# Optimization experiments

Hardware: AMD Instinct MI355X
Metric: run time of the kernel (lower is better)

## Reference

```python
import jax, jax.numpy as jnp
import numpy as np

B, S, C, O, H = 4, 4096, 2048, 2048, 8
DH = O // H  # per-head dim = 256
EPS = 1e-5


def setup_inputs() -> dict:
    key = jax.random.key(0)
    ks = jax.random.split(key, 12)
    init = lambda k, shape: (jax.random.normal(k, shape, dtype=jnp.float32) * 0.02)
    return {
        "x": jax.random.normal(ks[0], (B, S, C), dtype=jnp.float32),
        "Wq": init(ks[1], (C, O)), "bq": jnp.zeros((O,), jnp.float32),
        "Wk": init(ks[2], (C, O)), "bk": jnp.zeros((O,), jnp.float32),
        "Wv": init(ks[3], (C, O)), "bv": jnp.zeros((O,), jnp.float32),
        "Wo": init(ks[4], (O, C)), "bo": jnp.zeros((C,), jnp.float32),
        "gamma": jnp.ones((C,), jnp.float32),
        "beta": jnp.zeros((C,), jnp.float32),
    }


def reference(x, Wq, bq, Wk, bk, Wv, bv, Wo, bo, gamma, beta):
    b, s, _ = x.shape
    q = (x @ Wq + bq).reshape(b, s, H, DH)
    k = (x @ Wk + bk).reshape(b, s, H, DH)
    v = (x @ Wv + bv).reshape(b, s, H, DH)
    # As written in the source: matmul over the LAST two dims of [B,S,H,DH],
    # i.e. per-position attention across heads -> scores [B,S,H,H].
    scores = jnp.einsum("bshd,bstd->bsht", q, k) / jnp.sqrt(jnp.float32(DH))
    attn = jax.nn.softmax(scores, axis=-1)
    attended = jnp.einsum("bsht,bstd->bshd", attn, v).reshape(b, s, O)
    out = attended @ Wo + bo
    # residual + LayerNorm over the channel dim
    y = x + out
    mu = jnp.mean(y, axis=-1, keepdims=True)
    var = jnp.mean(jnp.square(y - mu), axis=-1, keepdims=True)
    return gamma * (y - mu) * jax.lax.rsqrt(var + EPS) + beta
```

## Files before the change

### kernel.cpp

```cpp
#include <hip/hip_runtime.h>
#include <hip/hip_bf16.h>
#include <stdint.h>


using short8  = __attribute__((ext_vector_type(8))) short;
using floatx4 = __attribute__((ext_vector_type(4))) float;

__device__ __forceinline__ float bf2f(ushort u) {
    union { uint32_t i; float f; } v; v.i = ((uint32_t)u) << 16; return v.f;
}
__device__ __forceinline__ ushort f2bf(float f) {
    union { float f; uint32_t i; } v; v.f = f;
    uint32_t r = v.i + 0x7fffu + ((v.i >> 16) & 1u);
    return (ushort)(r >> 16);
}
__device__ __forceinline__ short8 pack8(const floatx4& a, const floatx4& b) {
    short8 o;
    o[0] = (short)f2bf(a[0]); o[1] = (short)f2bf(a[1]);
    o[2] = (short)f2bf(a[2]); o[3] = (short)f2bf(a[3]);
    o[4] = (short)f2bf(b[0]); o[5] = (short)f2bf(b[1]);
    o[6] = (short)f2bf(b[2]); o[7] = (short)f2bf(b[3]);
    return o;
}
__device__ __forceinline__ void async_copy16(const void* g, void* l) {
    __builtin_amdgcn_global_load_lds(
        (__attribute__((address_space(1))) uint32_t*)g,
        (__attribute__((address_space(3))) uint32_t*)l,
        16, 0, 0);
}

#define GBAR do { asm volatile("" ::: "memory"); \
                  __builtin_amdgcn_s_barrier(); \
                  asm volatile("" ::: "memory"); } while (0)
#define LGKM0 asm volatile("s_waitcnt lgkmcnt(0)" ::: "memory")

__global__ void cvt_bf16(const float* __restrict__ in, ushort* __restrict__ out) {
    const size_t base = ((size_t)blockIdx.x * 256 + threadIdx.x) * 8;
    floatx4 a = *(const floatx4*)&in[base];
    floatx4 b = *(const floatx4*)&in[base + 4];
    *(short8*)&out[base] = pack8(a, b);
}

__global__ void convT2048(const float* __restrict__ in, ushort* __restrict__ out) {
    __shared__ alignas(16) float tile[32][33];
    const int x = blockIdx.x * 32 + threadIdx.x;
    const int y0 = blockIdx.y * 32;
    for (int j = threadIdx.y; j < 32; j += 8)
        tile[j][threadIdx.x] = in[(size_t)(y0 + j) * 2048 + x];
    __syncthreads();
    const int x2 = blockIdx.y * 32 + threadIdx.x;
    const int y2 = blockIdx.x * 32;
    for (int j = threadIdx.y; j < 32; j += 8)
        out[(size_t)(y2 + j) * 2048 + x2] = f2bf(tile[threadIdx.x][j]);
}

template <typename CT, int N>
__global__ __launch_bounds__(512, 2)
void gemm256(const ushort* __restrict__ A, int lda,
             const ushort* __restrict__ Bt,
             const float* __restrict__ b0, const float* __restrict__ b1,
             const float* __restrict__ b2,
             const float* __restrict__ resid, CT* __restrict__ C)
{
    constexpr int K   = 2048;
    constexpr int NKT = K / 64;
    constexpr int NT  = N / 256;
    constexpr int SW  = NT / 8;
    __shared__ alignas(16) ushort lA[2][256 * 64];
    __shared__ alignas(16) ushort lB[2][256 * 64];

    const int t    = threadIdx.x;
    const int wid  = t >> 6, lane = t & 63;
    const int wr   = wid >> 2, wc = wid & 3;
    const int lr   = lane & 15, q4 = lane >> 4;
    const int swk  = lr & 7;

    const int l    = (int)blockIdx.x;
    const int xcd  = l & 7;
    const int j2   = l >> 3;
    const int row0 = (j2 / SW) * 256;
    const int col0 = (xcd * SW + (j2 % SW)) * 256;

    const float* bias; int boff;
    if (col0 < 2048)      { bias = b0; boff = 0; }
    else if (col0 < 4096) { bias = b1; boff = 2048; }
    else                  { bias = b2; boff = 4096; }

    const int rpb = t >> 3;
    const int sp  = t & 7;
    const int gc0 = (sp ^ (rpb & 7)) * 8;
    const ushort* pA0 = A  + (size_t)(row0 + rpb)      * lda + gc0;
    const ushort* pA1 = A  + (size_t)(row0 + 64 + rpb) * lda + gc0;
    const ushort* pB0 = Bt + (size_t)(col0 + rpb)      * K   + gc0;
    const ushort* pB1 = Bt + (size_t)(col0 + 64 + rpb) * K   + gc0;

#define STAGE_A(buf, half, kn) do { \
    async_copy16(pA0 + (size_t)(half) * 128 * lda + (kn) * 64, \
                 &lA[buf][(half) * 8192 + t * 8]); \
    async_copy16(pA1 + (size_t)(half) * 128 * lda + (kn) * 64, \
                 &lA[buf][(half) * 8192 + 4096 + t * 8]); \
} while (0)
#define STAGE_B(buf, half, kn) do { \
    async_copy16(pB0 + (size_t)(half) * 128 * K + (kn) * 64, \
                 &lB[buf][(half) * 8192 + t * 8]); \
    async_copy16(pB1 + (size_t)(half) * 128 * K + (kn) * 64, \
                 &lB[buf][(half) * 8192 + 4096 + t * 8]); \
} while (0)

    const int arow = (wr * 128 + lr) * 64;
    const int brow = (wc * 64  + lr) * 64;
    const int c0 = ((0 + q4) ^ swk) * 8;
    const int c1 = ((4 + q4) ^ swk) * 8;

    floatx4 acc[8][4];
    #pragma unroll
    for (int i = 0; i < 8; i++)
        #pragma unroll
        for (int j = 0; j < 4; j++)
            acc[i][j] = (floatx4){0.f, 0.f, 0.f, 0.f};

    STAGE_A(0, 0, 0); STAGE_A(0, 1, 0);
    STAGE_B(0, 0, 0); STAGE_B(0, 1, 0);
    STAGE_A(1, 0, 1); STAGE_A(1, 1, 1);
    asm volatile("s_waitcnt vmcnt(4)" ::: "memory");
    GBAR;

    short8 af[8][2], bf[4][2];

    for (int kt = 0; kt < NKT; ++kt) {
        const int c = kt & 1;

        #pragma unroll
        for (int i = 0; i < 4; i++) {
            af[i][0] = *(const short8*)&lA[c][arow + i * 1024 + c0];
            af[i][1] = *(const short8*)&lA[c][arow + i * 1024 + c1];
        }
        #pragma unroll
        for (int j = 0; j < 2; j++) {
            bf[j][0] = *(const short8*)&lB[c][brow + j * 1024 + c0];
            bf[j][1] = *(const short8*)&lB[c][brow + j * 1024 + c1];
        }
        if (kt < NKT - 1) STAGE_B(c ^ 1, 0, kt + 1);
        GBAR; LGKM0;
        __builtin_amdgcn_s_setprio(1);
        #pragma unroll
        for (int i = 0; i < 4; i++)
            #pragma unroll
            for (int j = 0; j < 2; j++)
                #pragma unroll
                for (int ks = 0; ks < 2; ks++)
                    acc[i][j] = __builtin_amdgcn_mfma_f32_16x16x32_bf16(
                        af[i][ks], bf[j][ks], acc[i][j], 0, 0, 0);
        __builtin_amdgcn_s_setprio(0);
        GBAR;

        #pragma unroll
        for (int i = 4; i < 8; i++) {
            af[i][0] = *(const short8*)&lA[c][arow + i * 1024 + c0];
            af[i][1] = *(const short8*)&lA[c][arow + i * 1024 + c1];
        }
        #pragma unroll
        for (int j = 2; j < 4; j++) {
            bf[j][0] = *(const short8*)&lB[c][brow + j * 1024 + c0];
            bf[j][1] = *(const short8*)&lB[c][brow + j * 1024 + c1];
        }
        if (kt < NKT - 1) STAGE_B(c ^ 1, 1, kt + 1);
        GBAR; LGKM0;
        __builtin_amdgcn_s_setprio(1);
        #pragma unroll
        for (int i = 4; i < 8; i++)
            #pragma unroll
            for (int j = 2; j < 4; j++)
                #pragma unroll
                for (int ks = 0; ks < 2; ks++)
                    acc[i][j] = __builtin_amdgcn_mfma_f32_16x16x32_bf16(
                        af[i][ks], bf[j][ks], acc[i][j], 0, 0, 0);
        __builtin_amdgcn_s_setprio(0);
        GBAR;

        if (kt < NKT - 2) STAGE_A(c, 0, kt + 2);
        __builtin_amdgcn_s_setprio(1);
        #pragma unroll
        for (int i = 0; i < 4; i++)
            #pragma unroll
            for (int j = 2; j < 4; j++)
                #pragma unroll
                for (int ks = 0; ks < 2; ks++)
                    acc[i][j] = __builtin_amdgcn_mfma_f32_16x16x32_bf16(
                        af[i][ks], bf[j][ks], acc[i][j], 0, 0, 0);
        __builtin_amdgcn_s_setprio(0);
        GBAR;

        if (kt < NKT - 2) STAGE_A(c, 1, kt + 2);
        __builtin_amdgcn_s_setprio(1);
        #pragma unroll
        for (int i = 4; i < 8; i++)
            #pragma unroll
            for (int j = 0; j < 2; j++)
                #pragma unroll
                for (int ks = 0; ks < 2; ks++)
                    acc[i][j] = __builtin_amdgcn_mfma_f32_16x16x32_bf16(
                        af[i][ks], bf[j][ks], acc[i][j], 0, 0, 0);
        __builtin_amdgcn_s_setprio(0);
        if (kt < NKT - 2)       { asm volatile("s_waitcnt vmcnt(4)" ::: "memory"); }
        else if (kt == NKT - 2) { asm volatile("s_waitcnt vmcnt(0)" ::: "memory"); }
        if (kt < NKT - 1) GBAR;
    }
#undef STAGE_A
#undef STAGE_B

    #pragma unroll
    for (int j = 0; j < 4; j++) {
        const int gcol = col0 + wc * 64 + j * 16 + lr;
        const float bv = bias[gcol - boff];
        #pragma unroll
        for (int i = 0; i < 8; i++) {
            #pragma unroll
            for (int r = 0; r < 4; r++) {
                const int grow = row0 + wr * 128 + i * 16 + q4 * 4 + r;
                const size_t off = (size_t)grow * N + gcol;
                float v = acc[i][j][r] + bv;
                if (resid) v += resid[off];
                if constexpr (__is_same(CT, float)) C[off] = v;
                else                                C[off] = f2bf(v);
            }
        }
    }
}

template <int N>
__global__ __launch_bounds__(256, 2)
void gemm_f32a(const float* __restrict__ A, int lda,
               const ushort* __restrict__ Bt,
               const float* __restrict__ b0, const float* __restrict__ b1,
               const float* __restrict__ b2, ushort* __restrict__ C)
{
    constexpr int K = 2048;
    constexpr int NT = N / 128;
    constexpr int SW = NT / 8;
    __shared__ alignas(16) float  lA32[128 * 32];
    __shared__ alignas(16) ushort lB[128 * 32];

    const int t = threadIdx.x;
    const int wave = t >> 6, lane = t & 63;

    const int l = (int)blockIdx.x;
    const int xcd = l & 7;
    const int j2 = l >> 3;
    const int row0 = (j2 / SW) * 128;
    const int col0 = (xcd * SW + (j2 % SW)) * 128;

    const float* bias; int boff;
    if (col0 < 2048)      { bias = b0; boff = 0; }
    else if (col0 < 4096) { bias = b1; boff = 2048; }
    else                  { bias = b2; boff = 4096; }

    const int ar = t >> 3, ac = (t & 7) * 4;
    const float* gA0 = A + (size_t)(row0 + ar) * lda + ac;
    const ushort* gB0 = Bt + (size_t)(col0 + (t >> 2)) * K + (t & 3) * 8;
    const ushort* gB1 = Bt + (size_t)(col0 + 64 + (t >> 2)) * K + (t & 3) * 8;

    const int wm = (wave >> 1) * 64;
    const int wn = (wave & 1) * 64;
    const int q4 = lane >> 4;
    const int lr = lane & 15;

    floatx4 acc[4][4];
    #pragma unroll
    for (int i = 0; i < 4; i++)
        #pragma unroll
        for (int j = 0; j < 4; j++)
            acc[i][j] = (floatx4){0.f, 0.f, 0.f, 0.f};

    for (int kt = 0; kt < K / 32; ++kt) {
        const int ko = kt * 32;
        #pragma unroll
        for (int n = 0; n < 4; n++)
            async_copy16(gA0 + (size_t)n * 32 * lda + ko, &lA32[(n * 256 + t) * 4]);
        async_copy16(gB0 + ko, &lB[t * 8]);
        async_copy16(gB1 + ko, &lB[2048 + t * 8]);
        __syncthreads();

        short8 af[4], bfr[4];
        #pragma unroll
        for (int i = 0; i < 4; i++) {
            const floatx4* pa = (const floatx4*)&lA32[(wm + i * 16 + lr) * 32 + q4 * 8];
            af[i] = pack8(pa[0], pa[1]);
        }
        #pragma unroll
        for (int j = 0; j < 4; j++)
            bfr[j] = *(const short8*)&lB[(wn + j * 16 + lr) * 32 + q4 * 8];

        #pragma unroll
        for (int i = 0; i < 4; i++)
            #pragma unroll
            for (int j = 0; j < 4; j++)
                acc[i][j] = __builtin_amdgcn_mfma_f32_16x16x32_bf16(
                    af[i], bfr[j], acc[i][j], 0, 0, 0);
        __syncthreads();
    }

    #pragma unroll
    for (int j = 0; j < 4; j++) {
        const int gcol = col0 + wn + j * 16 + lr;
        const float bv = bias[gcol - boff];
        #pragma unroll
        for (int i = 0; i < 4; i++)
            #pragma unroll
            for (int r = 0; r < 4; r++) {
                const int grow = row0 + wm + i * 16 + q4 * 4 + r;
                C[(size_t)grow * N + gcol] = f2bf(acc[i][j][r] + bv);
            }
    }
}

__global__ __launch_bounds__(256, 2)
void attn_kernel(ushort* __restrict__ qkv)
{
    __shared__ alignas(16) ushort sq[4][2048];
    __shared__ alignas(16) ushort sk[4][2048];
    __shared__ alignas(16) ushort sv[4][2048];
    const int wave = threadIdx.x >> 6, lane = threadIdx.x & 63;
    const size_t p = (size_t)blockIdx.x * 4 + wave;
    const size_t base = p * 6144;

    #pragma unroll
    for (int c = 0; c < 4; c++) {
        const int idx = c * 512 + lane * 8;
        *(short8*)&sq[wave][idx] = *(const short8*)&qkv[base + idx];
        *(short8*)&sk[wave][idx] = *(const short8*)&qkv[base + 2048 + idx];
        *(short8*)&sv[wave][idx] = *(const short8*)&qkv[base + 4096 + idx];
    }

    const int h = lane >> 3;
    const int tt = lane & 7;
    float s = 0.f;
    #pragma unroll 4
    for (int c = 0; c < 32; c++) {
        short8 qv = *(const short8*)&sq[wave][h * 256 + c * 8];
        short8 kv = *(const short8*)&sk[wave][tt * 256 + c * 8];
        #pragma unroll
        for (int e = 0; e < 8; e++)
            s += bf2f((ushort)qv[e]) * bf2f((ushort)kv[e]);
    }
    s *= (1.0f / 16.0f);

    float m = s;
    m = fmaxf(m, __shfl_xor(m, 1));
    m = fmaxf(m, __shfl_xor(m, 2));
    m = fmaxf(m, __shfl_xor(m, 4));
    float e = __expf(s - m);
    float sum = e;
    sum += __shfl_xor(sum, 1);
    sum += __shfl_xor(sum, 2);
    sum += __shfl_xor(sum, 4);
    const float w = e / sum;

    float wt[8];
    #pragma unroll
    for (int t2 = 0; t2 < 8; t2++)
        wt[t2] = __shfl(w, (lane & 56) + t2);

    const int d0 = (lane & 7) * 8;
    #pragma unroll
    for (int c = 0; c < 4; c++) {
        const int d = d0 + c * 64;
        float acc[8] = {0, 0, 0, 0, 0, 0, 0, 0};
        #pragma unroll
        for (int t2 = 0; t2 < 8; t2++) {
            short8 vv = *(const short8*)&sv[wave][t2 * 256 + d];
            #pragma unroll
            for (int e2 = 0; e2 < 8; e2++)
                acc[e2] += wt[t2] * bf2f((ushort)vv[e2]);
        }
        short8 o;
        #pragma unroll
        for (int e2 = 0; e2 < 8; e2++)
            o[e2] = (short)f2bf(acc[e2]);
        *(short8*)&qkv[base + h * 256 + d] = o;
    }
}

__global__ __launch_bounds__(256, 2)
void ln_kernel(float* __restrict__ y, const float* __restrict__ gamma,
               const float* __restrict__ beta)
{
    __shared__ float red[2][4];
    const int t = threadIdx.x;
    const size_t base = (size_t)blockIdx.x * 2048 + t * 8;
    floatx4 a = *(const floatx4*)&y[base];
    floatx4 b = *(const floatx4*)&y[base + 4];
    float f[8] = {a[0], a[1], a[2], a[3], b[0], b[1], b[2], b[3]};
    float s = 0.f, ss = 0.f;
    #pragma unroll
    for (int e = 0; e < 8; e++) { s += f[e]; ss += f[e] * f[e]; }
    #pragma unroll
    for (int off = 1; off < 64; off <<= 1) {
        s  += __shfl_xor(s, off);
        ss += __shfl_xor(ss, off);
    }
    const int wave = t >> 6, lane = t & 63;
    if (lane == 0) { red[0][wave] = s; red[1][wave] = ss; }
    __syncthreads();
    s  = red[0][0] + red[0][1] + red[0][2] + red[0][3];
    ss = red[1][0] + red[1][1] + red[1][2] + red[1][3];
    const float mu  = s * (1.f / 2048.f);
    const float var = fmaxf(ss * (1.f / 2048.f) - mu * mu, 0.f);
    const float rs  = rsqrtf(var + 1e-5f);
    floatx4 g0 = *(const floatx4*)&gamma[t * 8];
    floatx4 g1 = *(const floatx4*)&gamma[t * 8 + 4];
    floatx4 b0 = *(const floatx4*)&beta[t * 8];
    floatx4 b1 = *(const floatx4*)&beta[t * 8 + 4];
    floatx4 o0, o1;
    #pragma unroll
    for (int e = 0; e < 4; e++) {
        o0[e] = g0[e] * (f[e] - mu) * rs + b0[e];
        o1[e] = g1[e] * (f[e + 4] - mu) * rs + b1[e];
    }
    *(floatx4*)&y[base]     = o0;
    *(floatx4*)&y[base + 4] = o1;
}

extern "C" void kernel_launch(void* const* d_in, const int* in_sizes, int n_in,
                              void* d_out, int out_size, void* d_ws, size_t ws_size,
                              hipStream_t stream)
{
    const float* x     = (const float*)d_in[0];
    const float* Wq    = (const float*)d_in[1];
    const float* bq    = (const float*)d_in[2];
    const float* Wk    = (const float*)d_in[3];
    const float* bk    = (const float*)d_in[4];
    const float* Wv    = (const float*)d_in[5];
    const float* bv    = (const float*)d_in[6];
    const float* Wo    = (const float*)d_in[7];
    const float* bo    = (const float*)d_in[8];
    const float* gamma = (const float*)d_in[9];
    const float* beta  = (const float*)d_in[10];
    float* out = (float*)d_out;

    char* ws = (char*)d_ws;
    const size_t MB = 1024 * 1024;
    ushort* WqkvT = (ushort*)(ws + 0 * MB);
    ushort* WoT   = (ushort*)(ws + 24 * MB);

    const bool bigws = ws_size >= 288 * MB;
    ushort* xbf = (ushort*)(ws + 32 * MB);
    ushort* qkv = (ushort*)(ws + (bigws ? 96 : 32) * MB);

    dim3 tb(32, 8), tg(64, 64);
    convT2048<<<tg, tb, 0, stream>>>(Wq, WqkvT);
    convT2048<<<tg, tb, 0, stream>>>(Wk, WqkvT + 2048 * 2048);
    convT2048<<<tg, tb, 0, stream>>>(Wv, WqkvT + 2 * 2048 * 2048);
    convT2048<<<tg, tb, 0, stream>>>(Wo, WoT);

    if (bigws) {
        cvt_bf16<<<16384, 256, 0, stream>>>(x, xbf);
        gemm256<ushort, 6144><<<1536, 512, 0, stream>>>(
            xbf, 2048, WqkvT, bq, bk, bv, nullptr, qkv);
    } else {
        gemm_f32a<6144><<<6144, 256, 0, stream>>>(
            x, 2048, WqkvT, bq, bk, bv, qkv);
    }

    attn_kernel<<<4096, 256, 0, stream>>>(qkv);

    gemm256<float, 2048><<<512, 512, 0, stream>>>(
        qkv, 6144, WoT, bo, bo, bo, x, out);

    ln_kernel<<<16384, 256, 0, stream>>>(out, gamma, beta);
}
```

Measured before the change: 1.041 ms.

## Restructure GEMM main loop into row-quarter phases interleaving LDS loads with MFMAs

The inner k-tile loop is reorganized from four quadrant-based MFMA phases into four row-quarter phases. All B fragments are loaded up front and A fragments are loaded one quarter at a time, overlapping with the previous quarter's MFMAs, with fewer explicit LGKM waits. The goal is to hide LDS read latency behind matrix math and to cut the A fragment register footprint. It relies on the compiler inserting correct lgkm waits, and it changes when the A staging for k+2 is issued, which could affect global load overlap.

```diff
diff --git a/kernel.cpp b/kernel.cpp
--- a/kernel.cpp
+++ b/kernel.cpp
@@ -125,82 +125,66 @@
     asm volatile("s_waitcnt vmcnt(4)" ::: "memory");
     GBAR;
 
-    short8 af[8][2], bf[4][2];
+    short8 bf[4][2];
+    short8 aq[4][2][2];
+
+#define LOAD_AQ(q) do { \
+    _Pragma("unroll") \
+    for (int m = 0; m < 2; m++) { \
+        aq[q][m][0] = *(const short8*)&lA[c][arow + ((q) * 2 + m) * 1024 + c0]; \
+        aq[q][m][1] = *(const short8*)&lA[c][arow + ((q) * 2 + m) * 1024 + c1]; \
+    } \
+} while (0)
+#define MFMA_Q(q) do { \
+    _Pragma("unroll") \
+    for (int m = 0; m < 2; m++) \
+        _Pragma("unroll") \
+        for (int j = 0; j < 4; j++) \
+            _Pragma("unroll") \
+            for (int ks = 0; ks < 2; ks++) \
+                acc[(q) * 2 + m][j] = __builtin_amdgcn_mfma_f32_16x16x32_bf16( \
+                    aq[q][m][ks], bf[j][ks], acc[(q) * 2 + m][j], 0, 0, 0); \
+} while (0)
 
     for (int kt = 0; kt < NKT; ++kt) {
         const int c = kt & 1;
 
-        #pragma unroll
-        for (int i = 0; i < 4; i++) {
-            af[i][0] = *(const short8*)&lA[c][arow + i * 1024 + c0];
-            af[i][1] = *(const short8*)&lA[c][arow + i * 1024 + c1];
-        }
         #pragma unroll
         for (int j = 0; j < 2; j++) {
             bf[j][0] = *(const short8*)&lB[c][brow + j * 1024 + c0];
             bf[j][1] = *(const short8*)&lB[c][brow + j * 1024 + c1];
         }
-        if (kt < NKT - 1) STAGE_B(c ^ 1, 0, kt + 1);
-        GBAR; LGKM0;
-        __builtin_amdgcn_s_setprio(1);
-        #pragma unroll
-        for (int i = 0; i < 4; i++)
-            #pragma unroll
-            for (int j = 0; j < 2; j++)
-                #pragma unroll
-                for (int ks = 0; ks < 2; ks++)
-                    acc[i][j] = __builtin_amdgcn_mfma_f32_16x16x32_bf16(
-                        af[i][ks], bf[j][ks], acc[i][j], 0, 0, 0);
-        __builtin_amdgcn_s_setprio(0);
-        GBAR;
-
-        #pragma unroll
-        for (int i = 4; i < 8; i++) {
-            af[i][0] = *(const short8*)&lA[c][arow + i * 1024 + c0];
-            af[i][1] = *(const short8*)&lA[c][arow + i * 1024 + c1];
-        }
+        LOAD_AQ(0);
         #pragma unroll
         for (int j = 2; j < 4; j++) {
             bf[j][0] = *(const short8*)&lB[c][brow + j * 1024 + c0];
             bf[j][1] = *(const short8*)&lB[c][brow + j * 1024 + c1];
         }
+        LOAD_AQ(1);
+        if (kt < NKT - 1) STAGE_B(c ^ 1, 0, kt + 1);
+        GBAR;
+        __builtin_amdgcn_s_setprio(1);
+        MFMA_Q(0);
+        __builtin_amdgcn_s_setprio(0);
+
+        LOAD_AQ(2);
         if (kt < NKT - 1) STAGE_B(c ^ 1, 1, kt + 1);
-        GBAR; LGKM0;
+        GBAR;
         __builtin_amdgcn_s_setprio(1);
-        #pragma unroll
-        for (int i = 4; i < 8; i++)
-            #pragma unroll
-            for (int j = 2; j < 4; j++)
-                #pragma unroll
-                for (int ks = 0; ks < 2; ks++)
-                    acc[i][j] = __builtin_amdgcn_mfma_f32_16x16x32_bf16(
-                        af[i][ks], bf[j][ks], acc[i][j], 0, 0, 0);
+        MFMA_Q(1);
         __builtin_amdgcn_s_setprio(0);
+
+        LOAD_AQ(3);
         GBAR;
-
-        if (kt < NKT - 2) STAGE_A(c, 0, kt + 2);
         __builtin_amdgcn_s_setprio(1);
-        #pragma unroll
-        for (int i = 0; i < 4; i++)
-            #pragma unroll
-            for (int j = 2; j < 4; j++)
-                #pragma unroll
-                for (int ks = 0; ks < 2; ks++)
-                    acc[i][j] = __builtin_amdgcn_mfma_f32_16x16x32_bf16(
-                        af[i][ks], bf[j][ks], acc[i][j], 0, 0, 0);
+        MFMA_Q(2);
         __builtin_amdgcn_s_setprio(0);
+
+        LGKM0;
         GBAR;
-
-        if (kt < NKT - 2) STAGE_A(c, 1, kt + 2);
+        if (kt < NKT - 2) { STAGE_A(c, 0, kt + 2); STAGE_A(c, 1, kt + 2); }
         __builtin_amdgcn_s_setprio(1);
-        #pragma unroll
-        for (int i = 4; i < 8; i++)
-            #pragma unroll
-            for (int j = 0; j < 2; j++)
-                #pragma unroll
-                for (int ks = 0; ks < 2; ks++)
-                    acc[i][j] = __builtin_amdgcn_mfma_f32_16x16x32_bf16(
-                        af[i][ks], bf[j][ks], acc[i][j], 0, 0, 0);
+        MFMA_Q(3);
         __builtin_amdgcn_s_setprio(0);
         if (kt < NKT - 2)       { asm volatile("s_waitcnt vmcnt(4)" ::: "memory"); }
         else if (kt == NKT - 2) { asm volatile("s_waitcnt vmcnt(0)" ::: "memory"); }
@@ -208,6 +192,8 @@
     }
 #undef STAGE_A
 #undef STAGE_B
+#undef LOAD_AQ
+#undef MFMA_Q
 
     #pragma unroll
     for (int j = 0; j < 4; j++) {
```

Result: no change. 1.028 ms (-1.3%).
